# Performance work log

Measured on AMD Instinct MI355X. Metric: run time of the kernel, lower is better.

The kernel has to match this reference:

```python
import jax, jax.numpy as jnp
import numpy as np

LENGTH = 320  # hard-coded in the layer
BIG = 1e5     # cap for 'no zero pixel in column' distances; BIG**2 = 1e10 -> exp() underflows to 0


def _edt_sq(zero):
    """Exact squared Euclidean distance transform.

    zero: [N, H, W] bool, True where the uint8-restored mask is 0 (seed pixels).
    Returns [N, H, W] float32 squared distance of every pixel to the nearest seed.
    Phase 1: 1D distance along H via associative scans (nearest seed above/below).
    Phase 2: exact lower envelope over W via a vectorized min-reduction:
             D2[n,i,j] = min_x ( (j-x)^2 + g2[n,i,x] ).
    """
    N, H, W = zero.shape
    ih = jnp.arange(H, dtype=jnp.float32)[None, :, None]            # [1,H,1]
    last = jax.lax.associative_scan(jnp.maximum,
                                    jnp.where(zero, ih, -BIG), axis=1)
    nxt = jax.lax.associative_scan(jnp.minimum,
                                   jnp.where(zero, ih, 2.0 * BIG), axis=1,
                                   reverse=True)
    g = jnp.minimum(jnp.minimum(ih - last, nxt - ih), BIG)           # [N,H,W] 1D dist
    g2 = g * g
    jw = jnp.arange(W, dtype=jnp.float32)
    off = (jw[:, None] - jw[None, :]) ** 2                           # [Wj, Wx]
    # [N,H,Wj,Wx] broadcast + min over source column x
    d2 = jnp.min(g2[:, :, None, :] + off[None, None], axis=-1)
    return d2


def _forward(inputs):
    B, H, W, _ = inputs.shape
    # uint8 cast: zero iff (1-x)*127.5 < 1  (matches tf.cast truncation)
    restored = ((1.0 - jax.lax.stop_gradient(inputs)) * 127.5).astype(jnp.uint8)
    zero = restored == 0                                             # [B,H,W,2]
    zm = jnp.moveaxis(zero, -1, 1).reshape(B * 2, H, W)              # fold channel into batch
    d2 = _edt_sq(zm).reshape(B, 2, H, W)
    sigmas = jnp.asarray([0.02, 0.08, 0.16], jnp.float32) * LENGTH   # [3]
    denom = 2.0 * sigmas * sigmas
    # exp(-d^2 / (2 sigma^2)) for each (channel, sigma); channel-major order like the loop
    clicks = jnp.exp(-d2[:, :, None] / denom[None, None, :, None, None])  # [B,2,3,H,W]
    return jnp.moveaxis(clicks.reshape(B, 6, H, W), 1, -1)          # [B,H,W,6]


def setup_inputs() -> dict:
    key = jax.random.key(0)
    inputs = jax.random.uniform(key, (4, 320, 320, 2), dtype=jnp.float32)
    return {"inputs": inputs}


def reference(inputs):
    return _forward(inputs)
```

## Files before the change

### kernel.cpp

```cpp
#include <hip/hip_runtime.h>

#define HH 320
#define WW 320
#define NIMG 8
#define BIGF 1.0e5f

#define TW  16
#define NCH 32
#define CH  10

__global__ __launch_bounds__(512) void edt_vert(const float* __restrict__ in,
                                                float* __restrict__ g2) {
    int wl = threadIdx.x;
    int ch = threadIdx.y;
    int b  = blockIdx.x / 20;
    int wt = blockIdx.x % 20;
    int w  = wt * TW + wl;
    int h0 = ch * CH;

    const float2* ip = (const float2*)in + (size_t)(b * HH + h0) * WW + w;
    float2 v[CH];
    #pragma unroll
    for (int k = 0; k < CH; ++k) v[k] = ip[(size_t)k * WW];

    unsigned m0 = 0, m1 = 0;
    #pragma unroll
    for (int k = 0; k < CH; ++k) {
        if ((1.0f - v[k].x) * 127.5f < 1.0f) m0 |= 1u << k;
        if ((1.0f - v[k].y) * 127.5f < 1.0f) m1 |= 1u << k;
    }

    __shared__ float sL[2][NCH][TW], sN[2][NCH][TW];
    sL[0][ch][wl] = m0 ? (float)(h0 + 31 - __clz((int)m0)) : -1.0e9f;
    sL[1][ch][wl] = m1 ? (float)(h0 + 31 - __clz((int)m1)) : -1.0e9f;
    sN[0][ch][wl] = m0 ? (float)(h0 + __ffs((int)m0) - 1)  :  1.0e9f;
    sN[1][ch][wl] = m1 ? (float)(h0 + __ffs((int)m1) - 1)  :  1.0e9f;
    __syncthreads();

    float L0 = -1.0e9f, L1 = -1.0e9f, N0 = 1.0e9f, N1 = 1.0e9f;
    for (int cc = 0; cc < NCH; ++cc) {
        float a0 = sL[0][cc][wl], a1 = sL[1][cc][wl];
        float b0 = sN[0][cc][wl], b1 = sN[1][cc][wl];
        if (cc < ch) { L0 = fmaxf(L0, a0); L1 = fmaxf(L1, a1); }
        if (cc > ch) { N0 = fminf(N0, b0); N1 = fminf(N1, b1); }
    }

    float gd0[CH], gd1[CH];
    float r0 = L0, r1 = L1;
    #pragma unroll
    for (int k = 0; k < CH; ++k) {
        float fh = (float)(h0 + k);
        if (m0 & (1u << k)) r0 = fh;
        if (m1 & (1u << k)) r1 = fh;
        gd0[k] = fh - r0;
        gd1[k] = fh - r1;
    }
    float* gp0 = g2 + ((size_t)(b * 2 + 0) * HH + h0) * WW + w;
    float* gp1 = g2 + ((size_t)(b * 2 + 1) * HH + h0) * WW + w;
    r0 = N0; r1 = N1;
    #pragma unroll
    for (int k = CH - 1; k >= 0; --k) {
        float fh = (float)(h0 + k);
        if (m0 & (1u << k)) r0 = fh;
        if (m1 & (1u << k)) r1 = fh;
        float g0 = fminf(fminf(gd0[k], r0 - fh), BIGF);
        float g1 = fminf(fminf(gd1[k], r1 - fh), BIGF);
        gp0[(size_t)k * WW] = g0 * g0;
        gp1[(size_t)k * WW] = g1 * g1;
    }
}

__global__ __launch_bounds__(256) void edt_horiz(const float* __restrict__ g2,
                                                 float* __restrict__ out) {
    int wv   = threadIdx.x >> 6;
    int lane = threadIdx.x & 63;
    int b  = blockIdx.x / 160;
    int hp = blockIdx.x % 160;
    int hh = wv >> 1;
    int c  = wv & 1;
    int row = (2 * b + c) * HH + (2 * hp + hh);

    __shared__ __align__(16) float sa[4][WW];
    __shared__ float sd2[2][2][WW];

    const float* grow = g2 + (size_t)row * WW;
    #pragma unroll
    for (int m = 0; m < 5; ++m) {
        int x = lane + 64 * m;
        float fx = (float)x;
        sa[wv][x] = fmaf(fx, fx, grow[x]);
    }

    const float4* sv = (const float4*)sa[wv];
    float d2v[5], n2j[5];
    #pragma unroll
    for (int m = 0; m < 5; ++m) {
        d2v[m] = 3.4e38f;
        n2j[m] = -2.0f * (float)(lane + 64 * m);
    }

    float4 cur[8], nxt[8];
    #pragma unroll
    for (int q = 0; q < 8; ++q) cur[q] = sv[q];
    #pragma unroll
    for (int t = 0; t < 10; ++t) {
        if (t < 9) {
            #pragma unroll
            for (int q = 0; q < 8; ++q) nxt[q] = sv[8 * (t + 1) + q];
        }
        #pragma unroll
        for (int q = 0; q < 8; ++q) {
            float a0 = cur[q].x, a1 = cur[q].y, a2 = cur[q].z, a3 = cur[q].w;
            float x0 = (float)(32 * t + 4 * q);
            #pragma unroll
            for (int m = 0; m < 5; ++m) {
                float t0 = fmaf(n2j[m], x0,        a0);
                float t1 = fmaf(n2j[m], x0 + 1.0f, a1);
                float t2 = fmaf(n2j[m], x0 + 2.0f, a2);
                float t3 = fmaf(n2j[m], x0 + 3.0f, a3);
                d2v[m] = fminf(fminf(d2v[m], fminf(t0, t1)), fminf(t2, t3));
            }
        }
        #pragma unroll
        for (int q = 0; q < 8; ++q) cur[q] = nxt[q];
    }

    #pragma unroll
    for (int m = 0; m < 5; ++m) {
        float fj = (float)(lane + 64 * m);
        sd2[hh][c][lane + 64 * m] = fmaf(fj, fj, d2v[m]);
    }
    __syncthreads();

    float* obase = out + (size_t)(b * HH + 2 * hp) * WW * 6;
    for (int q = threadIdx.x; q < 960; q += 256) {
        int D = 4 * q;
        int hh2 = D / 1920;
        int rr = D - 1920 * hh2;
        float vals[4];
        #pragma unroll
        for (int e = 0; e < 4; ++e) {
            int idx = rr + e;
            int jj = idx / 6;
            int cs = idx - 6 * jj;
            int c2 = (cs >= 3) ? 1 : 0;
            int s  = cs - 3 * c2;
            float dd = sd2[hh2][c2][jj];
            float co = (s == 0) ? (1.0f / 81.92f)
                     : (s == 1) ? (1.0f / 1310.72f)
                                : (1.0f / 5242.88f);
            vals[e] = __expf(-dd * co);
        }
        float4 o = {vals[0], vals[1], vals[2], vals[3]};
        *(float4*)(obase + D) = o;
    }
}

extern "C" void kernel_launch(void* const* d_in, const int* in_sizes, int n_in,
                              void* d_out, int out_size, void* d_ws, size_t ws_size,
                              hipStream_t stream) {
    const float* in = (const float*)d_in[0];
    float* out = (float*)d_out;
    float* g2 = (float*)d_ws;

    edt_vert<<<4 * 20, dim3(TW, NCH), 0, stream>>>(in, g2);
    edt_horiz<<<4 * 160, 256, 0, stream>>>(g2, out);
}
```

Measured before the change: 74.37 us.

## Split EDT work across more blocks: per-channel vertical, half-width horizontal

The vertical pass now launches one block per (image, channel, tile), which doubles the grid and halves per-thread register work. The horizontal pass gives each block a single row, and each wave handles half of the source columns. The two halves combine their partial minima through shared memory, which adds an extra barrier. The aim is more parallelism and occupancy on a GPU that was underfilled (80 and 640 blocks). The cost is redundant input loads and extra synchronization.

After: 73.72 us. Within noise of the previous version (-0.9%).

```diff
diff --git a/kernel.cpp b/kernel.cpp
--- a/kernel.cpp
+++ b/kernel.cpp
@@ -2,7 +2,6 @@
 
 #define HH 320
 #define WW 320
-#define NIMG 8
 #define BIGF 1.0e5f
 
 #define TW  16
@@ -13,82 +12,80 @@
                                                 float* __restrict__ g2) {
     int wl = threadIdx.x;
     int ch = threadIdx.y;
-    int b  = blockIdx.x / 20;
+    int bc = blockIdx.x / 20;
     int wt = blockIdx.x % 20;
+    int b  = bc >> 1;
+    int c  = bc & 1;
     int w  = wt * TW + wl;
     int h0 = ch * CH;
 
     const float2* ip = (const float2*)in + (size_t)(b * HH + h0) * WW + w;
-    float2 v[CH];
-    #pragma unroll
-    for (int k = 0; k < CH; ++k) v[k] = ip[(size_t)k * WW];
-
-    unsigned m0 = 0, m1 = 0;
+    float vv[CH];
     #pragma unroll
     for (int k = 0; k < CH; ++k) {
-        if ((1.0f - v[k].x) * 127.5f < 1.0f) m0 |= 1u << k;
-        if ((1.0f - v[k].y) * 127.5f < 1.0f) m1 |= 1u << k;
+        float2 t = ip[(size_t)k * WW];
+        vv[k] = c ? t.y : t.x;
     }
 
-    __shared__ float sL[2][NCH][TW], sN[2][NCH][TW];
-    sL[0][ch][wl] = m0 ? (float)(h0 + 31 - __clz((int)m0)) : -1.0e9f;
-    sL[1][ch][wl] = m1 ? (float)(h0 + 31 - __clz((int)m1)) : -1.0e9f;
-    sN[0][ch][wl] = m0 ? (float)(h0 + __ffs((int)m0) - 1)  :  1.0e9f;
-    sN[1][ch][wl] = m1 ? (float)(h0 + __ffs((int)m1) - 1)  :  1.0e9f;
+    unsigned m0 = 0;
+    #pragma unroll
+    for (int k = 0; k < CH; ++k)
+        if ((1.0f - vv[k]) * 127.5f < 1.0f) m0 |= 1u << k;
+
+    __shared__ float sL[NCH][TW], sN[NCH][TW];
+    sL[ch][wl] = m0 ? (float)(h0 + 31 - __clz((int)m0)) : -1.0e9f;
+    sN[ch][wl] = m0 ? (float)(h0 + __ffs((int)m0) - 1)  :  1.0e9f;
     __syncthreads();
 
-    float L0 = -1.0e9f, L1 = -1.0e9f, N0 = 1.0e9f, N1 = 1.0e9f;
+    float L0 = -1.0e9f, N0 = 1.0e9f;
     for (int cc = 0; cc < NCH; ++cc) {
-        float a0 = sL[0][cc][wl], a1 = sL[1][cc][wl];
-        float b0 = sN[0][cc][wl], b1 = sN[1][cc][wl];
-        if (cc < ch) { L0 = fmaxf(L0, a0); L1 = fmaxf(L1, a1); }
-        if (cc > ch) { N0 = fminf(N0, b0); N1 = fminf(N1, b1); }
+        float a0 = sL[cc][wl];
+        float b0 = sN[cc][wl];
+        if (cc < ch) L0 = fmaxf(L0, a0);
+        if (cc > ch) N0 = fminf(N0, b0);
     }
 
-    float gd0[CH], gd1[CH];
-    float r0 = L0, r1 = L1;
+    float gd0[CH];
+    float r0 = L0;
     #pragma unroll
     for (int k = 0; k < CH; ++k) {
         float fh = (float)(h0 + k);
         if (m0 & (1u << k)) r0 = fh;
-        if (m1 & (1u << k)) r1 = fh;
         gd0[k] = fh - r0;
-        gd1[k] = fh - r1;
     }
-    float* gp0 = g2 + ((size_t)(b * 2 + 0) * HH + h0) * WW + w;
-    float* gp1 = g2 + ((size_t)(b * 2 + 1) * HH + h0) * WW + w;
-    r0 = N0; r1 = N1;
+    float* gp0 = g2 + ((size_t)bc * HH + h0) * WW + w;
+    r0 = N0;
     #pragma unroll
     for (int k = CH - 1; k >= 0; --k) {
         float fh = (float)(h0 + k);
         if (m0 & (1u << k)) r0 = fh;
-        if (m1 & (1u << k)) r1 = fh;
         float g0 = fminf(fminf(gd0[k], r0 - fh), BIGF);
-        float g1 = fminf(fminf(gd1[k], r1 - fh), BIGF);
         gp0[(size_t)k * WW] = g0 * g0;
-        gp1[(size_t)k * WW] = g1 * g1;
     }
 }
 
-__global__ __launch_bounds__(256) void edt_horiz(const float* __restrict__ g2,
-                                                 float* __restrict__ out) {
+__global__ __launch_bounds__(256, 5) void edt_horiz(const float* __restrict__ g2,
+                                                    float* __restrict__ out) {
     int wv   = threadIdx.x >> 6;
     int lane = threadIdx.x & 63;
-    int b  = blockIdx.x / 160;
-    int hp = blockIdx.x % 160;
-    int hh = wv >> 1;
-    int c  = wv & 1;
-    int row = (2 * b + c) * HH + (2 * hp + hh);
+    int b    = blockIdx.x / HH;
+    int h    = blockIdx.x % HH;
+    int c    = wv >> 1;
+    int half = wv & 1;
+    int row  = (2 * b + c) * HH + h;
 
-    __shared__ __align__(16) float sa[4][WW];
-    __shared__ float sd2[2][2][WW];
+    __shared__ __align__(16) float sa[4][160];
+    __shared__ float pd[2][5][64];
+    __shared__ float sd2[2][WW];
 
-    const float* grow = g2 + (size_t)row * WW;
+    const float* grow = g2 + (size_t)row * WW + half * 160;
     #pragma unroll
-    for (int m = 0; m < 5; ++m) {
+    for (int m = 0; m < 3; ++m) {
         int x = lane + 64 * m;
-        float fx = (float)x;
-        sa[wv][x] = fmaf(fx, fx, grow[x]);
+        if (x < 160) {
+            float fx = (float)(x + half * 160);
+            sa[wv][x] = fmaf(fx, fx, grow[x]);
+        }
     }
 
     const float4* sv = (const float4*)sa[wv];
@@ -99,19 +96,16 @@
         n2j[m] = -2.0f * (float)(lane + 64 * m);
     }
 
-    float4 cur[8], nxt[8];
+    float xbase = (float)(half * 160);
     #pragma unroll
-    for (int q = 0; q < 8; ++q) cur[q] = sv[q];
-    #pragma unroll
-    for (int t = 0; t < 10; ++t) {
-        if (t < 9) {
-            #pragma unroll
-            for (int q = 0; q < 8; ++q) nxt[q] = sv[8 * (t + 1) + q];
-        }
+    for (int t = 0; t < 5; ++t) {
+        float4 cur[8];
+        #pragma unroll
+        for (int q = 0; q < 8; ++q) cur[q] = sv[8 * t + q];
         #pragma unroll
         for (int q = 0; q < 8; ++q) {
             float a0 = cur[q].x, a1 = cur[q].y, a2 = cur[q].z, a3 = cur[q].w;
-            float x0 = (float)(32 * t + 4 * q);
+            float x0 = xbase + (float)(32 * t + 4 * q);
             #pragma unroll
             for (int m = 0; m < 5; ++m) {
                 float t0 = fmaf(n2j[m], x0,        a0);
@@ -121,31 +115,35 @@
                 d2v[m] = fminf(fminf(d2v[m], fminf(t0, t1)), fminf(t2, t3));
             }
         }
-        #pragma unroll
-        for (int q = 0; q < 8; ++q) cur[q] = nxt[q];
     }
 
-    #pragma unroll
-    for (int m = 0; m < 5; ++m) {
-        float fj = (float)(lane + 64 * m);
-        sd2[hh][c][lane + 64 * m] = fmaf(fj, fj, d2v[m]);
+    if (half) {
+        #pragma unroll
+        for (int m = 0; m < 5; ++m) pd[c][m][lane] = d2v[m];
+    }
+    __syncthreads();
+    if (!half) {
+        #pragma unroll
+        for (int m = 0; m < 5; ++m) {
+            float dmin = fminf(d2v[m], pd[c][m][lane]);
+            float fj = (float)(lane + 64 * m);
+            sd2[c][lane + 64 * m] = fmaf(fj, fj, dmin);
+        }
     }
     __syncthreads();
 
-    float* obase = out + (size_t)(b * HH + 2 * hp) * WW * 6;
-    for (int q = threadIdx.x; q < 960; q += 256) {
+    float* obase = out + (size_t)(b * HH + h) * WW * 6;
+    for (int q = threadIdx.x; q < 480; q += 256) {
         int D = 4 * q;
-        int hh2 = D / 1920;
-        int rr = D - 1920 * hh2;
         float vals[4];
         #pragma unroll
         for (int e = 0; e < 4; ++e) {
-            int idx = rr + e;
+            int idx = D + e;
             int jj = idx / 6;
             int cs = idx - 6 * jj;
             int c2 = (cs >= 3) ? 1 : 0;
             int s  = cs - 3 * c2;
-            float dd = sd2[hh2][c2][jj];
+            float dd = sd2[c2][jj];
             float co = (s == 0) ? (1.0f / 81.92f)
                      : (s == 1) ? (1.0f / 1310.72f)
                                 : (1.0f / 5242.88f);
@@ -163,6 +161,6 @@
     float* out = (float*)d_out;
     float* g2 = (float*)d_ws;
 
-    edt_vert<<<4 * 20, dim3(TW, NCH), 0, stream>>>(in, g2);
-    edt_horiz<<<4 * 160, 256, 0, stream>>>(g2, out);
+    edt_vert<<<8 * 20, dim3(TW, NCH), 0, stream>>>(in, g2);
+    edt_horiz<<<4 * HH, 256, 0, stream>>>(g2, out);
 }
```
